# Kernel optimization log

Measured on AMD Instinct MI355X. Metric: run time of the kernel, lower is better.

## Reference

```python
import jax, jax.numpy as jnp
import numpy as np

N = 100000
E = 1600000
IN_C, HID_C, OUT_C = 64, 64, 16


def setup_inputs() -> dict:
    key = jax.random.key(0)
    k1, k2, k3, k4, k5 = jax.random.split(key, 5)
    x = jax.random.normal(k1, (N, IN_C), dtype=jnp.float32)
    edge_index = jax.random.randint(k2, (2, E), 0, N, dtype=jnp.int64)
    # Glorot-style init like PyG GCNConv
    W1 = jax.random.normal(k3, (IN_C, HID_C), dtype=jnp.float32) * (1.0 / np.sqrt(IN_C))
    b1 = jnp.zeros((HID_C,), dtype=jnp.float32)
    W2 = jax.random.normal(k4, (HID_C, OUT_C), dtype=jnp.float32) * (1.0 / np.sqrt(HID_C))
    b2 = jnp.zeros((OUT_C,), dtype=jnp.float32)
    return {"x": x, "edge_index": edge_index, "W1": W1, "b1": b1, "W2": W2, "b2": b2}


def _gcn_conv(h, src, dst, norm, W, b, n_nodes):
    # h: [N, F_in] -> linear transform first (PyG order), then normalized aggregation
    h = h @ W  # [N, F_out]
    msgs = h[src] * norm[:, None]          # gather + scale, [E+N, F_out]
    out = jax.ops.segment_sum(msgs, dst, num_segments=n_nodes)  # scatter-add
    return out + b


def reference(x, edge_index, W1, b1, W2, b2):
    n = x.shape[0]
    loop = jnp.arange(n, dtype=edge_index.dtype)
    src = jnp.concatenate([edge_index[0], loop])  # add self-loops
    dst = jnp.concatenate([edge_index[1], loop])
    # symmetric normalization D^{-1/2} (A+I) D^{-1/2}
    deg = jax.ops.segment_sum(jnp.ones_like(dst, dtype=x.dtype), dst, num_segments=n)
    dinv = jnp.where(deg > 0, jax.lax.rsqrt(deg), 0.0)
    norm = dinv[src] * dinv[dst]  # [E+N]

    h = jax.nn.relu(_gcn_conv(x, src, dst, norm, W1, b1, n))
    # dropout is identity in eval mode
    return _gcn_conv(h, src, dst, norm, W2, b2, n)
```

## Files before the change

### kernel.cpp

```cpp
#include <hip/hip_runtime.h>


namespace {
constexpr int BLK = 256;
constexpr int NPB = 256;
constexpr int PCHUNK = 8192;
constexpr int STRIDE = 5120;
constexpr int CPAD = 32;

__device__ inline float bf2f(unsigned short h) {
    union { unsigned u; float f; } v; v.u = (unsigned)h << 16; return v.f;
}
__device__ inline unsigned short f2bf(float f) {
    union { float f; unsigned u; } v; v.f = f;
    unsigned r = (v.u + 0x7FFFu + ((v.u >> 16) & 1u)) >> 16;
    return (unsigned short)r;
}
__device__ inline unsigned pack2bf(float a, float b) {
    return (unsigned)f2bf(a) | ((unsigned)f2bf(b) << 16);
}
__device__ inline int sel4(int s0, int s1, int s2, int s3, int q) {
    int sa = (q & 1) ? s1 : s0;
    int sb = (q & 1) ? s3 : s2;
    return (q & 2) ? sb : sa;
}

__device__ inline float gather8(const unsigned short* __restrict__ hhat,
                                const int* __restrict__ ssrc, int base, int lane) {
    int s0 = ssrc[base + 0], s1 = ssrc[base + 1];
    int s2 = ssrc[base + 2], s3 = ssrc[base + 3];
    int s4 = ssrc[base + 4], s5 = ssrc[base + 5];
    int s6 = ssrc[base + 6], s7 = ssrc[base + 7];
    float v0 = bf2f(hhat[((size_t)s0 << 6) + lane]);
    float v1 = bf2f(hhat[((size_t)s1 << 6) + lane]);
    float v2 = bf2f(hhat[((size_t)s2 << 6) + lane]);
    float v3 = bf2f(hhat[((size_t)s3 << 6) + lane]);
    float v4 = bf2f(hhat[((size_t)s4 << 6) + lane]);
    float v5 = bf2f(hhat[((size_t)s5 << 6) + lane]);
    float v6 = bf2f(hhat[((size_t)s6 << 6) + lane]);
    float v7 = bf2f(hhat[((size_t)s7 << 6) + lane]);
    return ((v0 + v1) + (v2 + v3)) + ((v4 + v5) + (v6 + v7));
}
__device__ inline float gather4(const unsigned short* __restrict__ hhat,
                                const int* __restrict__ ssrc, int base, int lane) {
    int s0 = ssrc[base + 0], s1 = ssrc[base + 1];
    int s2 = ssrc[base + 2], s3 = ssrc[base + 3];
    float v0 = bf2f(hhat[((size_t)s0 << 6) + lane]);
    float v1 = bf2f(hhat[((size_t)s1 << 6) + lane]);
    float v2 = bf2f(hhat[((size_t)s2 << 6) + lane]);
    float v3 = bf2f(hhat[((size_t)s3 << 6) + lane]);
    return (v0 + v1) + (v2 + v3);
}

__global__ __launch_bounds__(BLK) void k_zero(int* __restrict__ p, int n) {
    int i = blockIdx.x * BLK + threadIdx.x;
    if (i < n) p[i] = 0;
}

__global__ __launch_bounds__(BLK) void k_part(const int* __restrict__ src,
                                              const int* __restrict__ dst,
                                              int* __restrict__ bcnt,
                                              unsigned* __restrict__ packed,
                                              int e, int nb) {
    __shared__ int hist[1024];
    __shared__ int base[1024];
    int t = threadIdx.x;
    int chunk0 = blockIdx.x * PCHUNK;
    if (chunk0 >= e) return;
    int lim = min(PCHUNK, e - chunk0);
    int lim4 = lim >> 2;
    for (int i = t; i < nb; i += BLK) hist[i] = 0;
    __syncthreads();
    const int4* d4 = (const int4*)(dst + chunk0);
    for (int i = t; i < lim4; i += BLK) {
        int4 d = d4[i];
        atomicAdd(&hist[d.x >> 8], 1);
        atomicAdd(&hist[d.y >> 8], 1);
        atomicAdd(&hist[d.z >> 8], 1);
        atomicAdd(&hist[d.w >> 8], 1);
    }
    for (int i = (lim4 << 2) + t; i < lim; i += BLK)
        atomicAdd(&hist[dst[chunk0 + i] >> 8], 1);
    __syncthreads();
    for (int i = t; i < nb; i += BLK) {
        int c = hist[i];
        base[i] = c ? (i * STRIDE + atomicAdd(&bcnt[i * CPAD], c)) : 0;
        hist[i] = 0;
    }
    __syncthreads();
    const int4* s4 = (const int4*)(src + chunk0);
    for (int i = t; i < lim4; i += BLK) {
        int4 d = d4[i];
        int4 s = s4[i];
        int b0 = d.x >> 8, b1 = d.y >> 8, b2 = d.z >> 8, b3 = d.w >> 8;
        int r0 = atomicAdd(&hist[b0], 1);
        packed[base[b0] + r0] = ((unsigned)s.x << 8) | (unsigned)(d.x & 255);
        int r1 = atomicAdd(&hist[b1], 1);
        packed[base[b1] + r1] = ((unsigned)s.y << 8) | (unsigned)(d.y & 255);
        int r2 = atomicAdd(&hist[b2], 1);
        packed[base[b2] + r2] = ((unsigned)s.z << 8) | (unsigned)(d.z & 255);
        int r3 = atomicAdd(&hist[b3], 1);
        packed[base[b3] + r3] = ((unsigned)s.w << 8) | (unsigned)(d.w & 255);
    }
    for (int i = (lim4 << 2) + t; i < lim; i += BLK) {
        int d = dst[chunk0 + i];
        int b = d >> 8;
        int r = atomicAdd(&hist[b], 1);
        packed[base[b] + r] = ((unsigned)src[chunk0 + i] << 8) | (unsigned)(d & 255);
    }
}

__global__ __launch_bounds__(BLK) void k_sort(const unsigned* __restrict__ packed,
                                              const int* __restrict__ bcnt,
                                              int* __restrict__ ssrc,
                                              int* __restrict__ rowbeg,
                                              int* __restrict__ rowcnt,
                                              float* __restrict__ dinv, int n) {
    __shared__ unsigned sp[STRIDE];
    __shared__ int cnt[NPB];
    __shared__ int offs[NPB];
    int bid = blockIdx.x;
    int b = bid >> 2;
    int qr = bid & 3;
    int t = threadIdx.x;
    int regionBase = b * STRIDE;
    int ecnt = bcnt[b * CPAD];
    cnt[t] = 0;
    __syncthreads();
    for (int i = t; i < ecnt; i += BLK) {
        unsigned p = packed[regionBase + i];
        sp[i] = p;
        atomicAdd(&cnt[p & 255u], 1);
    }
    __syncthreads();
    int v = cnt[t];
    offs[t] = v;
    __syncthreads();
    for (int off = 1; off < NPB; off <<= 1) {
        int x = (t >= off) ? offs[t - off] : 0;
        __syncthreads();
        offs[t] += x;
        __syncthreads();
    }
    int myoff = offs[t] - v;
    int node = (b << 8) + t;
    if ((t >> 6) == qr && node < n) {
        rowbeg[node] = regionBase + myoff;
        rowcnt[node] = v;
        dinv[node] = rsqrtf((float)(v + 1));
    }
    __syncthreads();
    cnt[t] = regionBase + myoff;
    __syncthreads();
    int lo = qr << 6, hi = lo + 64;
    for (int i = t; i < ecnt; i += BLK) {
        unsigned p = sp[i];
        int dl = (int)(p & 255u);
        if (dl >= lo && dl < hi) {
            int pos = atomicAdd(&cnt[dl], 1);
            ssrc[pos] = (int)(p >> 8);
        }
    }
}


__global__ __launch_bounds__(BLK) void k_gemm1(const float* __restrict__ x,
                                               const float* __restrict__ W1,
                                               const float* __restrict__ dinv,
                                               unsigned short* __restrict__ hhat,
                                               int n, int ntiles) {
    __shared__ float W[64 * 64];
    int t = threadIdx.x;
    #pragma unroll
    for (int i = 0; i < 16; ++i) W[t + BLK * i] = W1[t + BLK * i];
    __syncthreads();
    const int cg = t & 3;
    const int ng = t >> 2;
    const float* Wc = W + cg * 16;

    for (int tile = blockIdx.x; tile < ntiles; tile += gridDim.x) {
        const int node0 = tile * 256 + ng * 4;
        int nd[4];
        #pragma unroll
        for (int i = 0; i < 4; ++i) {
            int v = node0 + i;
            nd[i] = (v < n) ? v : (n - 1);
        }
        float4 acc[4][4];
        #pragma unroll
        for (int i = 0; i < 4; ++i)
            #pragma unroll
            for (int c = 0; c < 4; ++c) acc[i][c] = make_float4(0.f, 0.f, 0.f, 0.f);

        for (int k4 = 0; k4 < 16; ++k4) {
            float4 xv[4];
            #pragma unroll
            for (int i = 0; i < 4; ++i)
                xv[i] = ((const float4*)(x + (size_t)nd[i] * 64))[k4];
            #pragma unroll
            for (int kk = 0; kk < 4; ++kk) {
                const float4* wr = (const float4*)(Wc + (k4 * 4 + kk) * 64);
                float4 w0 = wr[0], w1 = wr[1], w2 = wr[2], w3 = wr[3];
                #pragma unroll
                for (int i = 0; i < 4; ++i) {
                    float xa[4] = {xv[i].x, xv[i].y, xv[i].z, xv[i].w};
                    float xs = xa[kk];
                    acc[i][0].x = fmaf(xs, w0.x, acc[i][0].x);
                    acc[i][0].y = fmaf(xs, w0.y, acc[i][0].y);
                    acc[i][0].z = fmaf(xs, w0.z, acc[i][0].z);
                    acc[i][0].w = fmaf(xs, w0.w, acc[i][0].w);
                    acc[i][1].x = fmaf(xs, w1.x, acc[i][1].x);
                    acc[i][1].y = fmaf(xs, w1.y, acc[i][1].y);
                    acc[i][1].z = fmaf(xs, w1.z, acc[i][1].z);
                    acc[i][1].w = fmaf(xs, w1.w, acc[i][1].w);
                    acc[i][2].x = fmaf(xs, w2.x, acc[i][2].x);
                    acc[i][2].y = fmaf(xs, w2.y, acc[i][2].y);
                    acc[i][2].z = fmaf(xs, w2.z, acc[i][2].z);
                    acc[i][2].w = fmaf(xs, w2.w, acc[i][2].w);
                    acc[i][3].x = fmaf(xs, w3.x, acc[i][3].x);
                    acc[i][3].y = fmaf(xs, w3.y, acc[i][3].y);
                    acc[i][3].z = fmaf(xs, w3.z, acc[i][3].z);
                    acc[i][3].w = fmaf(xs, w3.w, acc[i][3].w);
                }
            }
        }
        #pragma unroll
        for (int i = 0; i < 4; ++i) {
            int v = node0 + i;
            if (v < n) {
                float d = dinv[v];
                unsigned u0 = pack2bf(acc[i][0].x * d, acc[i][0].y * d);
                unsigned u1 = pack2bf(acc[i][0].z * d, acc[i][0].w * d);
                unsigned u2 = pack2bf(acc[i][1].x * d, acc[i][1].y * d);
                unsigned u3 = pack2bf(acc[i][1].z * d, acc[i][1].w * d);
                unsigned u4 = pack2bf(acc[i][2].x * d, acc[i][2].y * d);
                unsigned u5 = pack2bf(acc[i][2].z * d, acc[i][2].w * d);
                unsigned u6 = pack2bf(acc[i][3].x * d, acc[i][3].y * d);
                unsigned u7 = pack2bf(acc[i][3].z * d, acc[i][3].w * d);
                uint4* dst = (uint4*)(hhat + (size_t)v * 64 + cg * 16);
                dst[0] = make_uint4(u0, u1, u2, u3);
                dst[1] = make_uint4(u4, u5, u6, u7);
            }
        }
    }
}

__global__ __launch_bounds__(BLK) void k_agg1(const unsigned short* __restrict__ hhat,
                                              const int* __restrict__ rowbeg,
                                              const int* __restrict__ rowcnt,
                                              const int* __restrict__ ssrc,
                                              const float* __restrict__ dinv,
                                              const float* __restrict__ b1,
                                              const float* __restrict__ W2,
                                              unsigned short* __restrict__ h2hat, int n) {
    int pair = __builtin_amdgcn_readfirstlane(
        (int)((blockIdx.x * BLK + threadIdx.x) >> 6));
    int lane = threadIdx.x & 63;
    int wid0 = pair << 1;
    if (wid0 >= n) return;
    int wid1 = wid0 + 1;
    bool has1 = (wid1 < n);
    const int g = lane >> 4;
    const int j = lane & 15;
    float w2r[16];
    #pragma unroll
    for (int k = 0; k < 16; ++k) w2r[k] = W2[(g * 16 + k) * 16 + j];

    int beg0 = rowbeg[wid0], cnt0 = rowcnt[wid0];
    int beg1 = 0, cnt1 = 0;
    if (has1) { beg1 = rowbeg[wid1]; cnt1 = rowcnt[wid1]; }
    float a0 = bf2f(hhat[((size_t)wid0 << 6) + lane]);
    float a1 = 0.f;
    if (has1) a1 = bf2f(hhat[((size_t)wid1 << 6) + lane]);
    int e0 = 0, e1 = 0;
    while (e0 + 8 <= cnt0 && e1 + 8 <= cnt1) {
        float r0 = gather8(hhat, ssrc, beg0 + e0, lane);
        float r1 = gather8(hhat, ssrc, beg1 + e1, lane);
        a0 += r0;
        a1 += r1;
        e0 += 8; e1 += 8;
    }
    for (; e0 + 8 <= cnt0; e0 += 8) a0 += gather8(hhat, ssrc, beg0 + e0, lane);
    for (; e1 + 8 <= cnt1; e1 += 8) a1 += gather8(hhat, ssrc, beg1 + e1, lane);
    if (e0 + 4 <= cnt0) { a0 += gather4(hhat, ssrc, beg0 + e0, lane); e0 += 4; }
    if (e1 + 4 <= cnt1) { a1 += gather4(hhat, ssrc, beg1 + e1, lane); e1 += 4; }
    for (; e0 < cnt0; ++e0) a0 += bf2f(hhat[((size_t)ssrc[beg0 + e0] << 6) + lane]);
    for (; e1 < cnt1; ++e1) a1 += bf2f(hhat[((size_t)ssrc[beg1 + e1] << 6) + lane]);

    {
        float dv = dinv[wid0];
        float h = fmaxf(fmaf(dv, a0, b1[lane]), 0.f);
        float part = 0.f;
        #pragma unroll
        for (int k = 0; k < 16; ++k)
            part = fmaf(__shfl(h, g * 16 + k, 64), w2r[k], part);
        part += __shfl_xor(part, 16, 64);
        part += __shfl_xor(part, 32, 64);
        if (g == 0) h2hat[(size_t)wid0 * 16 + j] = f2bf(part * dv);
    }
    if (has1) {
        float dv = dinv[wid1];
        float h = fmaxf(fmaf(dv, a1, b1[lane]), 0.f);
        float part = 0.f;
        #pragma unroll
        for (int k = 0; k < 16; ++k)
            part = fmaf(__shfl(h, g * 16 + k, 64), w2r[k], part);
        part += __shfl_xor(part, 16, 64);
        part += __shfl_xor(part, 32, 64);
        if (g == 0) h2hat[(size_t)wid1 * 16 + j] = f2bf(part * dv);
    }
}

__global__ __launch_bounds__(BLK) void k_agg2(const unsigned short* __restrict__ h2,
                                              const int* __restrict__ rowbeg,
                                              const int* __restrict__ rowcnt,
                                              const int* __restrict__ ssrc,
                                              const float* __restrict__ dinv,
                                              const float* __restrict__ b2,
                                              float* __restrict__ out, int n) {
    int pair = __builtin_amdgcn_readfirstlane(
        (int)((blockIdx.x * BLK + threadIdx.x) >> 6));
    int lane = threadIdx.x & 63;
    int w0 = pair << 1;
    if (w0 >= n) return;
    int w1 = w0 + 1;
    bool has1 = (w1 < n);
    int q = lane >> 4;
    int c = lane & 15;
    int beg0 = rowbeg[w0], cnt0 = rowcnt[w0];
    int beg1 = 0, cnt1 = 0;
    if (has1) { beg1 = rowbeg[w1]; cnt1 = rowcnt[w1]; }
    float a0 = 0.f, a1 = 0.f;
    int e0 = 0, e1 = 0;
    while (e0 + 8 <= cnt0 && e1 + 8 <= cnt1) {
        int p0 = beg0 + e0, p1 = beg1 + e1;
        int x0 = ssrc[p0 + 0], x1 = ssrc[p0 + 1], x2 = ssrc[p0 + 2], x3 = ssrc[p0 + 3];
        int x4 = ssrc[p0 + 4], x5 = ssrc[p0 + 5], x6 = ssrc[p0 + 6], x7 = ssrc[p0 + 7];
        int y0 = ssrc[p1 + 0], y1 = ssrc[p1 + 1], y2 = ssrc[p1 + 2], y3 = ssrc[p1 + 3];
        int y4 = ssrc[p1 + 4], y5 = ssrc[p1 + 5], y6 = ssrc[p1 + 6], y7 = ssrc[p1 + 7];
        int sA0 = sel4(x0, x1, x2, x3, q), sB0 = sel4(x4, x5, x6, x7, q);
        int sA1 = sel4(y0, y1, y2, y3, q), sB1 = sel4(y4, y5, y6, y7, q);
        float vA0 = bf2f(h2[((size_t)sA0 << 4) + c]);
        float vB0 = bf2f(h2[((size_t)sB0 << 4) + c]);
        float vA1 = bf2f(h2[((size_t)sA1 << 4) + c]);
        float vB1 = bf2f(h2[((size_t)sB1 << 4) + c]);
        a0 += vA0 + vB0;
        a1 += vA1 + vB1;
        e0 += 8; e1 += 8;
    }
    for (; e0 + 8 <= cnt0; e0 += 8) {
        int p0 = beg0 + e0;
        int x0 = ssrc[p0 + 0], x1 = ssrc[p0 + 1], x2 = ssrc[p0 + 2], x3 = ssrc[p0 + 3];
        int x4 = ssrc[p0 + 4], x5 = ssrc[p0 + 5], x6 = ssrc[p0 + 6], x7 = ssrc[p0 + 7];
        int sA = sel4(x0, x1, x2, x3, q), sB = sel4(x4, x5, x6, x7, q);
        a0 += bf2f(h2[((size_t)sA << 4) + c]) + bf2f(h2[((size_t)sB << 4) + c]);
    }
    if (e0 + 4 <= cnt0) {
        int p0 = beg0 + e0;
        int x0 = ssrc[p0 + 0], x1 = ssrc[p0 + 1], x2 = ssrc[p0 + 2], x3 = ssrc[p0 + 3];
        a0 += bf2f(h2[((size_t)sel4(x0, x1, x2, x3, q) << 4) + c]);
        e0 += 4;
    }
    if (e0 + q < cnt0)
        a0 += bf2f(h2[((size_t)ssrc[beg0 + e0 + q] << 4) + c]);
    for (; e1 + 8 <= cnt1; e1 += 8) {
        int p1 = beg1 + e1;
        int y0 = ssrc[p1 + 0], y1 = ssrc[p1 + 1], y2 = ssrc[p1 + 2], y3 = ssrc[p1 + 3];
        int y4 = ssrc[p1 + 4], y5 = ssrc[p1 + 5], y6 = ssrc[p1 + 6], y7 = ssrc[p1 + 7];
        int sA = sel4(y0, y1, y2, y3, q), sB = sel4(y4, y5, y6, y7, q);
        a1 += bf2f(h2[((size_t)sA << 4) + c]) + bf2f(h2[((size_t)sB << 4) + c]);
    }
    if (has1 && e1 + 4 <= cnt1) {
        int p1 = beg1 + e1;
        int y0 = ssrc[p1 + 0], y1 = ssrc[p1 + 1], y2 = ssrc[p1 + 2], y3 = ssrc[p1 + 3];
        a1 += bf2f(h2[((size_t)sel4(y0, y1, y2, y3, q) << 4) + c]);
        e1 += 4;
    }
    if (has1 && e1 + q < cnt1)
        a1 += bf2f(h2[((size_t)ssrc[beg1 + e1 + q] << 4) + c]);

    a0 += __shfl_xor(a0, 16, 64);
    a0 += __shfl_xor(a0, 32, 64);
    a1 += __shfl_xor(a1, 16, 64);
    a1 += __shfl_xor(a1, 32, 64);
    if (q == 0) {
        float self0 = bf2f(h2[((size_t)w0 << 4) + c]);
        out[((size_t)w0 << 4) + c] = fmaf(dinv[w0], a0 + self0, b2[c]);
        if (has1) {
            float self1 = bf2f(h2[((size_t)w1 << 4) + c]);
            out[((size_t)w1 << 4) + c] = fmaf(dinv[w1], a1 + self1, b2[c]);
        }
    }
}

}

extern "C" void kernel_launch(void* const* d_in, const int* in_sizes, int n_in,
                              void* d_out, int out_size, void* d_ws, size_t ws_size,
                              hipStream_t stream) {
    const float* x  = (const float*)d_in[0];
    const int*   ei = (const int*)d_in[1];
    const float* W1 = (const float*)d_in[2];
    const float* b1 = (const float*)d_in[3];
    const float* W2 = (const float*)d_in[4];
    const float* b2 = (const float*)d_in[5];
    float* out = (float*)d_out;

    const int N = in_sizes[0] / 64;
    const int E = in_sizes[1] / 2;
    const int* src = ei;
    const int* dst = ei + E;
    const int nb = (N + NPB - 1) / NPB;

    char* ws = (char*)d_ws;
    size_t off = 0;
    auto alloc = [&](size_t bytes) -> char* {
        char* p = ws + off;
        off = (off + bytes + 255) & ~(size_t)255;
        return p;
    };
    int*            bcnt   = (int*)alloc((size_t)1024 * CPAD * 4);
    int*            rowbeg = (int*)alloc((size_t)N * 4);
    int*            rowcnt = (int*)alloc((size_t)N * 4);
    float*          dinv   = (float*)alloc((size_t)N * 4);
    unsigned*       packed = (unsigned*)alloc((size_t)nb * STRIDE * 4);
    int*            ssrc   = (int*)alloc((size_t)nb * STRIDE * 4);
    unsigned short* hhat   = (unsigned short*)alloc((size_t)N * 64 * 2);
    unsigned short* h2hat  = (unsigned short*)alloc((size_t)N * 16 * 2);

    const int ntiles = (N + 255) / 256;
    const int g1grid = (ntiles < 1024) ? ntiles : 1024;
    const int nchunks = (E + PCHUNK - 1) / PCHUNK;
    const int npairs = (N + 1) / 2;
    const int nb_p = (int)(((long long)npairs * 64 + BLK - 1) / BLK);

    const int zn = nb * CPAD;
    k_zero<<<(zn + BLK - 1) / BLK, BLK, 0, stream>>>(bcnt, zn);
    k_part<<<nchunks, BLK, 0, stream>>>(src, dst, bcnt, packed, E, nb);
    k_sort<<<nb * 4, BLK, 0, stream>>>(packed, bcnt, ssrc, rowbeg, rowcnt, dinv, N);

    k_gemm1<<<g1grid, BLK, 0, stream>>>(x, W1, dinv, hhat, N, ntiles);
    k_agg1<<<nb_p, BLK, 0, stream>>>(hhat, rowbeg, rowcnt, ssrc, dinv, b1, W2,
                                     h2hat, N);
    k_agg2<<<nb_p, BLK, 0, stream>>>(h2hat, rowbeg, rowcnt, ssrc, dinv, b2, out, N);
}
```

Before: 200.3 us.

## Run sort and first GEMM in one launch, apply source dinv during gather

The sort and the first linear transform now run in a single launch with disjoint block ranges and a shared-memory union. To remove the GEMM's dependence on dinv, the source-side normalization moves out of the GEMM and into the aggregation, where each gathered row is scaled by dinv[src]. The zeroing kernel is replaced by hipMemsetAsync. This saves a launch and lets the GEMM overlap the sort, but it adds a scattered dinv load per edge in agg1 and raises LDS use for the GEMM blocks.

```diff
diff --git a/kernel.cpp b/kernel.cpp
--- a/kernel.cpp
+++ b/kernel.cpp
@@ -26,11 +26,15 @@
 }
 
 __device__ inline float gather8(const unsigned short* __restrict__ hhat,
-                                const int* __restrict__ ssrc, int base, int lane) {
+                                const int* __restrict__ ssrc,
+                                const float* __restrict__ dinv,
+                                int base, int lane) {
     int s0 = ssrc[base + 0], s1 = ssrc[base + 1];
     int s2 = ssrc[base + 2], s3 = ssrc[base + 3];
     int s4 = ssrc[base + 4], s5 = ssrc[base + 5];
     int s6 = ssrc[base + 6], s7 = ssrc[base + 7];
+    float d0 = dinv[s0], d1 = dinv[s1], d2 = dinv[s2], d3 = dinv[s3];
+    float d4 = dinv[s4], d5 = dinv[s5], d6 = dinv[s6], d7 = dinv[s7];
     float v0 = bf2f(hhat[((size_t)s0 << 6) + lane]);
     float v1 = bf2f(hhat[((size_t)s1 << 6) + lane]);
     float v2 = bf2f(hhat[((size_t)s2 << 6) + lane]);
@@ -39,22 +43,26 @@
     float v5 = bf2f(hhat[((size_t)s5 << 6) + lane]);
     float v6 = bf2f(hhat[((size_t)s6 << 6) + lane]);
     float v7 = bf2f(hhat[((size_t)s7 << 6) + lane]);
-    return ((v0 + v1) + (v2 + v3)) + ((v4 + v5) + (v6 + v7));
+    float t0 = fmaf(d1, v1, d0 * v0);
+    float t1 = fmaf(d3, v3, d2 * v2);
+    float t2 = fmaf(d5, v5, d4 * v4);
+    float t3 = fmaf(d7, v7, d6 * v6);
+    return (t0 + t1) + (t2 + t3);
 }
 __device__ inline float gather4(const unsigned short* __restrict__ hhat,
-                                const int* __restrict__ ssrc, int base, int lane) {
+                                const int* __restrict__ ssrc,
+                                const float* __restrict__ dinv,
+                                int base, int lane) {
     int s0 = ssrc[base + 0], s1 = ssrc[base + 1];
     int s2 = ssrc[base + 2], s3 = ssrc[base + 3];
+    float d0 = dinv[s0], d1 = dinv[s1], d2 = dinv[s2], d3 = dinv[s3];
     float v0 = bf2f(hhat[((size_t)s0 << 6) + lane]);
     float v1 = bf2f(hhat[((size_t)s1 << 6) + lane]);
     float v2 = bf2f(hhat[((size_t)s2 << 6) + lane]);
     float v3 = bf2f(hhat[((size_t)s3 << 6) + lane]);
-    return (v0 + v1) + (v2 + v3);
-}
-
-__global__ __launch_bounds__(BLK) void k_zero(int* __restrict__ p, int n) {
-    int i = blockIdx.x * BLK + threadIdx.x;
-    if (i < n) p[i] = 0;
+    float t0 = fmaf(d1, v1, d0 * v0);
+    float t1 = fmaf(d3, v3, d2 * v2);
+    return t0 + t1;
 }
 
 __global__ __launch_bounds__(BLK) void k_part(const int* __restrict__ src,
@@ -110,140 +118,137 @@
     }
 }
 
-__global__ __launch_bounds__(BLK) void k_sort(const unsigned* __restrict__ packed,
-                                              const int* __restrict__ bcnt,
-                                              int* __restrict__ ssrc,
-                                              int* __restrict__ rowbeg,
-                                              int* __restrict__ rowcnt,
-                                              float* __restrict__ dinv, int n) {
-    __shared__ unsigned sp[STRIDE];
-    __shared__ int cnt[NPB];
-    __shared__ int offs[NPB];
-    int bid = blockIdx.x;
-    int b = bid >> 2;
-    int qr = bid & 3;
+union SMemU {
+    struct { unsigned sp[STRIDE]; int cnt[NPB]; int offs[NPB]; } s;
+    float W[64 * 64];
+};
+
+__global__ __launch_bounds__(BLK) void k_sortgemm(
+    const unsigned* __restrict__ packed, const int* __restrict__ bcnt,
+    int* __restrict__ ssrc, int* __restrict__ rowbeg, int* __restrict__ rowcnt,
+    float* __restrict__ dinv, int n, int nsort,
+    const float* __restrict__ x, const float* __restrict__ W1,
+    unsigned short* __restrict__ hhat, int ntiles) {
+    __shared__ SMemU sm;
     int t = threadIdx.x;
-    int regionBase = b * STRIDE;
-    int ecnt = bcnt[b * CPAD];
-    cnt[t] = 0;
-    __syncthreads();
-    for (int i = t; i < ecnt; i += BLK) {
-        unsigned p = packed[regionBase + i];
-        sp[i] = p;
-        atomicAdd(&cnt[p & 255u], 1);
-    }
-    __syncthreads();
-    int v = cnt[t];
-    offs[t] = v;
-    __syncthreads();
-    for (int off = 1; off < NPB; off <<= 1) {
-        int x = (t >= off) ? offs[t - off] : 0;
-        __syncthreads();
-        offs[t] += x;
-        __syncthreads();
-    }
-    int myoff = offs[t] - v;
-    int node = (b << 8) + t;
-    if ((t >> 6) == qr && node < n) {
-        rowbeg[node] = regionBase + myoff;
-        rowcnt[node] = v;
-        dinv[node] = rsqrtf((float)(v + 1));
-    }
-    __syncthreads();
-    cnt[t] = regionBase + myoff;
-    __syncthreads();
-    int lo = qr << 6, hi = lo + 64;
-    for (int i = t; i < ecnt; i += BLK) {
-        unsigned p = sp[i];
-        int dl = (int)(p & 255u);
-        if (dl >= lo && dl < hi) {
-            int pos = atomicAdd(&cnt[dl], 1);
-            ssrc[pos] = (int)(p >> 8);
-        }
-    }
-}
-
-
-__global__ __launch_bounds__(BLK) void k_gemm1(const float* __restrict__ x,
-                                               const float* __restrict__ W1,
-                                               const float* __restrict__ dinv,
-                                               unsigned short* __restrict__ hhat,
-                                               int n, int ntiles) {
-    __shared__ float W[64 * 64];
-    int t = threadIdx.x;
-    #pragma unroll
-    for (int i = 0; i < 16; ++i) W[t + BLK * i] = W1[t + BLK * i];
-    __syncthreads();
-    const int cg = t & 3;
-    const int ng = t >> 2;
-    const float* Wc = W + cg * 16;
-
-    for (int tile = blockIdx.x; tile < ntiles; tile += gridDim.x) {
-        const int node0 = tile * 256 + ng * 4;
-        int nd[4];
+    if ((int)blockIdx.x < nsort) {
+        int bid = blockIdx.x;
+        int b = bid >> 2;
+        int qr = bid & 3;
+        int regionBase = b * STRIDE;
+        int ecnt = bcnt[b * CPAD];
+        sm.s.cnt[t] = 0;
+        __syncthreads();
+        for (int i = t; i < ecnt; i += BLK) {
+            unsigned p = packed[regionBase + i];
+            sm.s.sp[i] = p;
+            atomicAdd(&sm.s.cnt[p & 255u], 1);
+        }
+        __syncthreads();
+        int v = sm.s.cnt[t];
+        sm.s.offs[t] = v;
+        __syncthreads();
+        for (int off = 1; off < NPB; off <<= 1) {
+            int xx = (t >= off) ? sm.s.offs[t - off] : 0;
+            __syncthreads();
+            sm.s.offs[t] += xx;
+            __syncthreads();
+        }
+        int myoff = sm.s.offs[t] - v;
+        int node = (b << 8) + t;
+        if ((t >> 6) == qr && node < n) {
+            rowbeg[node] = regionBase + myoff;
+            rowcnt[node] = v;
+            dinv[node] = rsqrtf((float)(v + 1));
+        }
+        __syncthreads();
+        sm.s.cnt[t] = regionBase + myoff;
+        __syncthreads();
+        int lo = qr << 6, hi = lo + 64;
+        for (int i = t; i < ecnt; i += BLK) {
+            unsigned p = sm.s.sp[i];
+            int dl = (int)(p & 255u);
+            if (dl >= lo && dl < hi) {
+                int pos = atomicAdd(&sm.s.cnt[dl], 1);
+                ssrc[pos] = (int)(p >> 8);
+            }
+        }
+    } else {
         #pragma unroll
-        for (int i = 0; i < 4; ++i) {
-            int v = node0 + i;
-            nd[i] = (v < n) ? v : (n - 1);
-        }
-        float4 acc[4][4];
-        #pragma unroll
-        for (int i = 0; i < 4; ++i)
+        for (int i = 0; i < 16; ++i) sm.W[t + BLK * i] = W1[t + BLK * i];
+        __syncthreads();
+        const int cg = t & 3;
+        const int ng = t >> 2;
+        const float* Wc = sm.W + cg * 16;
+        const int g1grid = gridDim.x - nsort;
+
+        for (int tile = blockIdx.x - nsort; tile < ntiles; tile += g1grid) {
+            const int node0 = tile * 256 + ng * 4;
+            int nd[4];
             #pragma unroll
-            for (int c = 0; c < 4; ++c) acc[i][c] = make_float4(0.f, 0.f, 0.f, 0.f);
-
-        for (int k4 = 0; k4 < 16; ++k4) {
-            float4 xv[4];
+            for (int i = 0; i < 4; ++i) {
+                int vv = node0 + i;
+                nd[i] = (vv < n) ? vv : (n - 1);
+            }
+            float4 acc[4][4];
             #pragma unroll
             for (int i = 0; i < 4; ++i)
-                xv[i] = ((const float4*)(x + (size_t)nd[i] * 64))[k4];
-            #pragma unroll
-            for (int kk = 0; kk < 4; ++kk) {
-                const float4* wr = (const float4*)(Wc + (k4 * 4 + kk) * 64);
-                float4 w0 = wr[0], w1 = wr[1], w2 = wr[2], w3 = wr[3];
                 #pragma unroll
-                for (int i = 0; i < 4; ++i) {
-                    float xa[4] = {xv[i].x, xv[i].y, xv[i].z, xv[i].w};
-                    float xs = xa[kk];
-                    acc[i][0].x = fmaf(xs, w0.x, acc[i][0].x);
-                    acc[i][0].y = fmaf(xs, w0.y, acc[i][0].y);
-                    acc[i][0].z = fmaf(xs, w0.z, acc[i][0].z);
-                    acc[i][0].w = fmaf(xs, w0.w, acc[i][0].w);
-                    acc[i][1].x = fmaf(xs, w1.x, acc[i][1].x);
-                    acc[i][1].y = fmaf(xs, w1.y, acc[i][1].y);
-                    acc[i][1].z = fmaf(xs, w1.z, acc[i][1].z);
-                    acc[i][1].w = fmaf(xs, w1.w, acc[i][1].w);
-                    acc[i][2].x = fmaf(xs, w2.x, acc[i][2].x);
-                    acc[i][2].y = fmaf(xs, w2.y, acc[i][2].y);
-                    acc[i][2].z = fmaf(xs, w2.z, acc[i][2].z);
-                    acc[i][2].w = fmaf(xs, w2.w, acc[i][2].w);
-                    acc[i][3].x = fmaf(xs, w3.x, acc[i][3].x);
-                    acc[i][3].y = fmaf(xs, w3.y, acc[i][3].y);
-                    acc[i][3].z = fmaf(xs, w3.z, acc[i][3].z);
-                    acc[i][3].w = fmaf(xs, w3.w, acc[i][3].w);
+                for (int c = 0; c < 4; ++c) acc[i][c] = make_float4(0.f, 0.f, 0.f, 0.f);
+
+            for (int k4 = 0; k4 < 16; ++k4) {
+                float4 xv[4];
+                #pragma unroll
+                for (int i = 0; i < 4; ++i)
+                    xv[i] = ((const float4*)(x + (size_t)nd[i] * 64))[k4];
+                #pragma unroll
+                for (int kk = 0; kk < 4; ++kk) {
+                    const float4* wr = (const float4*)(Wc + (k4 * 4 + kk) * 64);
+                    float4 w0 = wr[0], w1 = wr[1], w2 = wr[2], w3 = wr[3];
+                    #pragma unroll
+                    for (int i = 0; i < 4; ++i) {
+                        float xa[4] = {xv[i].x, xv[i].y, xv[i].z, xv[i].w};
+                        float xs = xa[kk];
+                        acc[i][0].x = fmaf(xs, w0.x, acc[i][0].x);
+                        acc[i][0].y = fmaf(xs, w0.y, acc[i][0].y);
+                        acc[i][0].z = fmaf(xs, w0.z, acc[i][0].z);
+                        acc[i][0].w = fmaf(xs, w0.w, acc[i][0].w);
+                        acc[i][1].x = fmaf(xs, w1.x, acc[i][1].x);
+                        acc[i][1].y = fmaf(xs, w1.y, acc[i][1].y);
+                        acc[i][1].z = fmaf(xs, w1.z, acc[i][1].z);
+                        acc[i][1].w = fmaf(xs, w1.w, acc[i][1].w);
+                        acc[i][2].x = fmaf(xs, w2.x, acc[i][2].x);
+                        acc[i][2].y = fmaf(xs, w2.y, acc[i][2].y);
+                        acc[i][2].z = fmaf(xs, w2.z, acc[i][2].z);
+                        acc[i][2].w = fmaf(xs, w2.w, acc[i][2].w);
+                        acc[i][3].x = fmaf(xs, w3.x, acc[i][3].x);
+                        acc[i][3].y = fmaf(xs, w3.y, acc[i][3].y);
+                        acc[i][3].z = fmaf(xs, w3.z, acc[i][3].z);
+                        acc[i][3].w = fmaf(xs, w3.w, acc[i][3].w);
+                    }
                 }
             }
-        }
-        #pragma unroll
-        for (int i = 0; i < 4; ++i) {
-            int v = node0 + i;
-            if (v < n) {
-                float d = dinv[v];
-                unsigned u0 = pack2bf(acc[i][0].x * d, acc[i][0].y * d);
-                unsigned u1 = pack2bf(acc[i][0].z * d, acc[i][0].w * d);
-                unsigned u2 = pack2bf(acc[i][1].x * d, acc[i][1].y * d);
-                unsigned u3 = pack2bf(acc[i][1].z * d, acc[i][1].w * d);
-                unsigned u4 = pack2bf(acc[i][2].x * d, acc[i][2].y * d);
-                unsigned u5 = pack2bf(acc[i][2].z * d, acc[i][2].w * d);
-                unsigned u6 = pack2bf(acc[i][3].x * d, acc[i][3].y * d);
-                unsigned u7 = pack2bf(acc[i][3].z * d, acc[i][3].w * d);
-                uint4* dst = (uint4*)(hhat + (size_t)v * 64 + cg * 16);
-                dst[0] = make_uint4(u0, u1, u2, u3);
-                dst[1] = make_uint4(u4, u5, u6, u7);
+            #pragma unroll
+            for (int i = 0; i < 4; ++i) {
+                int vv = node0 + i;
+                if (vv < n) {
+                    unsigned u0 = pack2bf(acc[i][0].x, acc[i][0].y);
+                    unsigned u1 = pack2bf(acc[i][0].z, acc[i][0].w);
+                    unsigned u2 = pack2bf(acc[i][1].x, acc[i][1].y);
+                    unsigned u3 = pack2bf(acc[i][1].z, acc[i][1].w);
+                    unsigned u4 = pack2bf(acc[i][2].x, acc[i][2].y);
+                    unsigned u5 = pack2bf(acc[i][2].z, acc[i][2].w);
+                    unsigned u6 = pack2bf(acc[i][3].x, acc[i][3].y);
+                    unsigned u7 = pack2bf(acc[i][3].z, acc[i][3].w);
+                    uint4* dstp = (uint4*)(hhat + (size_t)vv * 64 + cg * 16);
+                    dstp[0] = make_uint4(u0, u1, u2, u3);
+                    dstp[1] = make_uint4(u4, u5, u6, u7);
+                }
             }
         }
     }
 }
+
 
 __global__ __launch_bounds__(BLK) void k_agg1(const unsigned short* __restrict__ hhat,
                                               const int* __restrict__ rowbeg,
@@ -269,23 +274,29 @@
     int beg0 = rowbeg[wid0], cnt0 = rowcnt[wid0];
     int beg1 = 0, cnt1 = 0;
     if (has1) { beg1 = rowbeg[wid1]; cnt1 = rowcnt[wid1]; }
-    float a0 = bf2f(hhat[((size_t)wid0 << 6) + lane]);
+    float a0 = dinv[wid0] * bf2f(hhat[((size_t)wid0 << 6) + lane]);
     float a1 = 0.f;
-    if (has1) a1 = bf2f(hhat[((size_t)wid1 << 6) + lane]);
+    if (has1) a1 = dinv[wid1] * bf2f(hhat[((size_t)wid1 << 6) + lane]);
     int e0 = 0, e1 = 0;
     while (e0 + 8 <= cnt0 && e1 + 8 <= cnt1) {
-        float r0 = gather8(hhat, ssrc, beg0 + e0, lane);
-        float r1 = gather8(hhat, ssrc, beg1 + e1, lane);
+        float r0 = gather8(hhat, ssrc, dinv, beg0 + e0, lane);
+        float r1 = gather8(hhat, ssrc, dinv, beg1 + e1, lane);
         a0 += r0;
         a1 += r1;
         e0 += 8; e1 += 8;
     }
-    for (; e0 + 8 <= cnt0; e0 += 8) a0 += gather8(hhat, ssrc, beg0 + e0, lane);
-    for (; e1 + 8 <= cnt1; e1 += 8) a1 += gather8(hhat, ssrc, beg1 + e1, lane);
-    if (e0 + 4 <= cnt0) { a0 += gather4(hhat, ssrc, beg0 + e0, lane); e0 += 4; }
-    if (e1 + 4 <= cnt1) { a1 += gather4(hhat, ssrc, beg1 + e1, lane); e1 += 4; }
-    for (; e0 < cnt0; ++e0) a0 += bf2f(hhat[((size_t)ssrc[beg0 + e0] << 6) + lane]);
-    for (; e1 < cnt1; ++e1) a1 += bf2f(hhat[((size_t)ssrc[beg1 + e1] << 6) + lane]);
+    for (; e0 + 8 <= cnt0; e0 += 8) a0 += gather8(hhat, ssrc, dinv, beg0 + e0, lane);
+    for (; e1 + 8 <= cnt1; e1 += 8) a1 += gather8(hhat, ssrc, dinv, beg1 + e1, lane);
+    if (e0 + 4 <= cnt0) { a0 += gather4(hhat, ssrc, dinv, beg0 + e0, lane); e0 += 4; }
+    if (e1 + 4 <= cnt1) { a1 += gather4(hhat, ssrc, dinv, beg1 + e1, lane); e1 += 4; }
+    for (; e0 < cnt0; ++e0) {
+        int s = ssrc[beg0 + e0];
+        a0 = fmaf(dinv[s], bf2f(hhat[((size_t)s << 6) + lane]), a0);
+    }
+    for (; e1 < cnt1; ++e1) {
+        int s = ssrc[beg1 + e1];
+        a1 = fmaf(dinv[s], bf2f(hhat[((size_t)s << 6) + lane]), a1);
+    }
 
     {
         float dv = dinv[wid0];
@@ -433,13 +444,14 @@
     const int nchunks = (E + PCHUNK - 1) / PCHUNK;
     const int npairs = (N + 1) / 2;
     const int nb_p = (int)(((long long)npairs * 64 + BLK - 1) / BLK);
+    const int nsort = nb * 4;
 
     const int zn = nb * CPAD;
-    k_zero<<<(zn + BLK - 1) / BLK, BLK, 0, stream>>>(bcnt, zn);
+    hipMemsetAsync(bcnt, 0, (size_t)zn * 4, stream);
     k_part<<<nchunks, BLK, 0, stream>>>(src, dst, bcnt, packed, E, nb);
-    k_sort<<<nb * 4, BLK, 0, stream>>>(packed, bcnt, ssrc, rowbeg, rowcnt, dinv, N);
-
-    k_gemm1<<<g1grid, BLK, 0, stream>>>(x, W1, dinv, hhat, N, ntiles);
+    k_sortgemm<<<nsort + g1grid, BLK, 0, stream>>>(packed, bcnt, ssrc, rowbeg,
+                                                   rowcnt, dinv, N, nsort,
+                                                   x, W1, hhat, ntiles);
     k_agg1<<<nb_p, BLK, 0, stream>>>(hhat, rowbeg, rowcnt, ssrc, dinv, b1, W2,
                                      h2hat, N);
     k_agg2<<<nb_p, BLK, 0, stream>>>(h2hat, rowbeg, rowcnt, ssrc, dinv, b2, out, N);
```

Result: slower. 217.9 us (+8.8%).
